# Kernel optimization log

Measured on AMD Instinct MI355X. Metric: run time of the kernel, lower is better.

The kernel has to match this reference:

```python
import jax, jax.numpy as jnp
import numpy as np

B, T, I, H, L, O = 8192, 204, 5, 24, 10, 612

def setup_inputs() -> dict:
    key = jax.random.key(0)
    ks = jax.random.split(key, 10)
    s_ih = 1.0 / np.sqrt(H)
    inp = {
        "x": jax.random.normal(ks[0], (B, T, I), dtype=jnp.float32),
        # torch nn.LSTM params: weight_ih_l0 [4H,I], weight_hh_l0 [4H,H], biases [4H]
        "W_ih": jax.random.uniform(ks[1], (4 * H, I), jnp.float32, -s_ih, s_ih),
        "W_hh": jax.random.uniform(ks[2], (4 * H, H), jnp.float32, -s_ih, s_ih),
        "b_ih": jax.random.uniform(ks[3], (4 * H,), jnp.float32, -s_ih, s_ih),
        "b_hh": jax.random.uniform(ks[4], (4 * H,), jnp.float32, -s_ih, s_ih),
        "fc0_w": jax.random.uniform(ks[5], (L, H * T), jnp.float32, -1 / np.sqrt(H * T), 1 / np.sqrt(H * T)),
        "fc0_b": jax.random.uniform(ks[6], (L,), jnp.float32, -1 / np.sqrt(H * T), 1 / np.sqrt(H * T)),
        "out_w": jax.random.uniform(ks[7], (O, L), jnp.float32, -1 / np.sqrt(L), 1 / np.sqrt(L)),
        "out_b": jax.random.uniform(ks[8], (O,), jnp.float32, -1 / np.sqrt(L), 1 / np.sqrt(L)),
    }
    return inp

def _lstm_forward(x, W_ih, W_hh, b_ih, b_hh):
    # Precompute input projections for all timesteps: [B,T,4H] -> time-major [T,B,4H]
    x_proj = jnp.einsum("bti,gi->btg", x, W_ih) + b_ih
    x_proj = jnp.swapaxes(x_proj, 0, 1)
    h0 = jnp.zeros((x.shape[0], W_hh.shape[1]), x.dtype)
    c0 = jnp.zeros_like(h0)

    def step(carry, xt):
        h, c = carry
        gates = xt + h @ W_hh.T + b_hh  # [B,4H]; torch gate order i,f,g,o
        i, f, g, o = jnp.split(gates, 4, axis=-1)
        c = jax.nn.sigmoid(f) * c + jax.nn.sigmoid(i) * jnp.tanh(g)
        h = jax.nn.sigmoid(o) * jnp.tanh(c)
        return (h, c), h

    _, hs = jax.lax.scan(step, (h0, c0), x_proj)  # hs: [T,B,H]
    return jnp.swapaxes(hs, 0, 1)  # [B,T,H]

def reference(x, W_ih, W_hh, b_ih, b_hh, fc0_w, fc0_b, out_w, out_b):
    h = _lstm_forward(x, W_ih, W_hh, b_ih, b_hh)       # [B,T,H]
    h = h.reshape(h.shape[0], -1)                       # [B, T*H]
    h = jax.nn.relu(h @ fc0_w.T + fc0_b)                # [B, L]
    return h @ out_w.T + out_b                          # [B, O]
```

## Files before the change

kernel.cpp:

```cpp
#include <hip/hip_runtime.h>
#include <math.h>

#define T_  204
#define I_  5
#define H_  24
#define L_  10
#define O_  612
#define Bsz 8192

typedef _Float16 half8 __attribute__((ext_vector_type(8)));
typedef _Float16 half2t __attribute__((ext_vector_type(2)));
typedef float    float4t __attribute__((ext_vector_type(4)));

union U16B { float4t f4; half8 h8; float f[4]; _Float16 h[8]; half2t h2[4]; };

__device__ __forceinline__ float fast_rcp(float x){ return __builtin_amdgcn_rcpf(x); }
__device__ __forceinline__ float fast_ex2(float x){ return __builtin_amdgcn_exp2f(x); }
__device__ __forceinline__ half2t pk2(float a, float b){
    return __builtin_bit_cast(half2t, __builtin_amdgcn_cvt_pkrtz(a, b));
}

#define MFMA16(a,b,c) __builtin_amdgcn_mfma_f32_16x16x32_f16((a),(b),(c),0,0,0)

#define L2E  1.44269504f
#define L2E2 2.88539008f

__device__ __forceinline__ float sigm2(float x){
    return fast_rcp(1.f + fast_ex2(x * -L2E));
}
__device__ __forceinline__ float tanh2(float x){
    return 2.f * fast_rcp(1.f + fast_ex2(x * -L2E2)) - 1.f;
}

__global__ __launch_bounds__(64)
void pack_fc0(const float* __restrict__ fc0_w, float4t* __restrict__ dst)
{
    const int t = blockIdx.x, lane = threadIdx.x;
    const int m = lane & 15, q = lane >> 4;
    U16B v;
    #pragma unroll
    for (int i = 0; i < 8; ++i) {
        const int k = 8*q + i;
        float f = (m < L_ && k < H_) ? fc0_w[m*(T_*H_) + t*H_ + k] : 0.0f;
        v.h[i] = (_Float16)f;
    }
    dst[t*64 + lane] = v.f4;
}

__global__ __launch_bounds__(64)
void lstm_mfma(const float* __restrict__ x,
               const float* __restrict__ W_ih,
               const float* __restrict__ W_hh,
               const float* __restrict__ b_ih,
               const float* __restrict__ b_hh,
               const float* __restrict__ fc0_b,
               const float* __restrict__ out_w,
               const float* __restrict__ out_b,
               const float4t* __restrict__ fc0A,
               float* __restrict__ out)
{
    __shared__ __align__(16) _Float16 hL[16*40];
    __shared__ __align__(16) _Float16 actL[16*24];

    const int lane = threadIdx.x;
    const int m = lane & 15;
    const int q = lane >> 4;
    const int elem = blockIdx.x * 16 + m;

    const float4t zf4 = {0.f, 0.f, 0.f, 0.f};

    half8 Ag[6];
    const int g0 = m & 3, ub = 6 * (m >> 2);
    #pragma unroll
    for (int T6 = 0; T6 < 6; ++T6) {
        const int srow = g0 * H_ + ub + T6;
        float w[8];
        if (q < 3) {
            const float4t* pw = (const float4t*)(W_hh + srow*H_ + 8*q);
            float4t wa = pw[0], wb = pw[1];
            #pragma unroll
            for (int i = 0; i < 4; ++i) { w[i] = wa[i]; w[4+i] = wb[i]; }
        } else {
            #pragma unroll
            for (int i = 0; i < 8; ++i) w[i] = 0.f;
            #pragma unroll
            for (int i = 0; i < I_; ++i) w[i] = W_ih[srow*I_ + i];
            w[5] = b_ih[srow] + b_hh[srow];
        }
        U16B tw;
        #pragma unroll
        for (int i = 0; i < 8; ++i) tw.h[i] = (_Float16)w[i];
        Ag[T6] = tw.h8;
    }

    const int hwAddr = m*40 + 6*q;
    const int hrAddr = m*40 + 8*q;

    const float* xp = x + (size_t)elem * (T_*I_);

    U16B B;
    if (q < 3) B.f4 = zf4;
    else {
        B.h2[0] = pk2(xp[0], xp[1]);
        B.h2[1] = pk2(xp[2], xp[3]);
        B.h2[2] = pk2(xp[4], 1.0f);
        B.h2[3] = pk2(0.f, 0.f);
    }
    float c_[6];
    #pragma unroll
    for (int s = 0; s < 6; ++s) c_[s] = 0.f;
    float4t accF = zf4;
    float4t fa = fc0A[lane];

    for (int t = 0; t < T_; ++t) {
        const int tn = (t + 1 < T_) ? t + 1 : t;
        const float4t fan = fc0A[tn*64 + lane];
        float xn0=0.f, xn1=0.f, xn2=0.f, xn3=0.f, xn4=0.f;
        if (q == 3) {
            const float* xq = xp + tn*I_;
            xn0 = xq[0]; xn1 = xq[1]; xn2 = xq[2]; xn3 = xq[3]; xn4 = xq[4];
        }

        float4t D0 = MFMA16(Ag[0], B.h8, zf4);
        float4t D1 = MFMA16(Ag[1], B.h8, zf4);
        float4t D2 = MFMA16(Ag[2], B.h8, zf4);
        float4t D3 = MFMA16(Ag[3], B.h8, zf4);
        float4t D4 = MFMA16(Ag[4], B.h8, zf4);
        float4t D5 = MFMA16(Ag[5], B.h8, zf4);

        float hh[6];
        {
            float4t D[6] = {D0, D1, D2, D3, D4, D5};
            #pragma unroll
            for (int T6 = 0; T6 < 6; ++T6) {
                const float si = sigm2(D[T6][0]);
                const float sf = sigm2(D[T6][1]);
                const float tg = tanh2(D[T6][2]);
                const float so = sigm2(D[T6][3]);
                c_[T6] = fmaf(sf, c_[T6], si * tg);
                hh[T6] = so * tanh2(c_[T6]);
            }
        }

        *(half2t*)(&hL[hwAddr])     = pk2(hh[0], hh[1]);
        *(half2t*)(&hL[hwAddr + 2]) = pk2(hh[2], hh[3]);
        *(half2t*)(&hL[hwAddr + 4]) = pk2(hh[4], hh[5]);
        __builtin_amdgcn_wave_barrier();

        if (q < 3) {
            B.f4 = *(const float4t*)(&hL[hrAddr]);
        } else {
            B.h2[0] = pk2(xn0, xn1);
            B.h2[1] = pk2(xn2, xn3);
            B.h2[2] = pk2(xn4, 1.0f);
            B.h2[3] = pk2(0.f, 0.f);
        }

        U16B fA; fA.f4 = fa;
        accF = MFMA16(fA.h8, B.h8, accF);
        fa = fan;
    }

    float av[4];
    #pragma unroll
    for (int r = 0; r < 4; ++r) {
        const int l = 4*q + r;
        const float fb = (l < L_) ? fc0_b[l] : 0.f;
        const float v = accF[r] + fb;
        av[r] = (l < L_) ? fmaxf(v, 0.f) : 0.f;
    }
    *(half2t*)(&actL[m*24 + 4*q])     = pk2(av[0], av[1]);
    *(half2t*)(&actL[m*24 + 4*q + 2]) = pk2(av[2], av[3]);
    __builtin_amdgcn_wave_barrier();

    U16B Ba;
    if (q < 2) Ba.f4 = *(const float4t*)(&actL[m*24 + q*8]);
    else       Ba.f4 = zf4;

    for (int Tt = 0; Tt < 39; ++Tt) {
        const int row = 16*Tt + m;
        float w0=0.f,w1=0.f,w2=0.f,w3=0.f,w4=0.f,w5=0.f,w6=0.f,w7=0.f;
        if (row < O_ && q < 2) {
            const float2* p2 = (const float2*)(out_w + row*L_);
            if (q == 0) {
                float2 a = p2[0], b = p2[1], cc = p2[2], dd = p2[3];
                w0=a.x; w1=a.y; w2=b.x; w3=b.y; w4=cc.x; w5=cc.y; w6=dd.x; w7=dd.y;
            } else {
                float2 a = p2[4];
                w0=a.x; w1=a.y;
            }
        }
        U16B Aw;
        Aw.h2[0] = pk2(w0,w1); Aw.h2[1] = pk2(w2,w3);
        Aw.h2[2] = pk2(w4,w5); Aw.h2[3] = pk2(w6,w7);

        float4t dd = MFMA16(Aw.h8, Ba.h8, zf4);

        const int ob = 16*Tt + 4*q;
        if (ob < O_) {
            const float4t bias = *(const float4t*)(out_b + ob);
            #pragma unroll
            for (int r = 0; r < 4; ++r) dd[r] += bias[r];
            *(float4t*)(out + (size_t)elem*O_ + ob) = dd;
        }
    }
}

extern "C" void kernel_launch(void* const* d_in, const int* in_sizes, int n_in,
                              void* d_out, int out_size, void* d_ws, size_t ws_size,
                              hipStream_t stream)
{
    const float* x     = (const float*)d_in[0];
    const float* W_ih  = (const float*)d_in[1];
    const float* W_hh  = (const float*)d_in[2];
    const float* b_ih  = (const float*)d_in[3];
    const float* b_hh  = (const float*)d_in[4];
    const float* fc0_w = (const float*)d_in[5];
    const float* fc0_b = (const float*)d_in[6];
    const float* out_w = (const float*)d_in[7];
    const float* out_b = (const float*)d_in[8];
    float* out = (float*)d_out;
    (void)ws_size;

    pack_fc0<<<dim3(T_), dim3(64), 0, stream>>>(fc0_w, (float4t*)d_ws);
    lstm_mfma<<<dim3(Bsz/16), dim3(64), 0, stream>>>(
        x, W_ih, W_hh, b_ih, b_hh, fc0_b, out_w, out_b,
        (const float4t*)d_ws, out);
}
```

Baseline: 224.4 us.

## Split LSTM gate tiles across two waves with double-buffered LDS and drop fc0 pack kernel

Each 16-element batch block now runs on two waves. Each wave computes three of the six gate MFMA tiles and half of the fc0 outputs, and the waves exchange h through a double-buffered LDS array with a workgroup barrier every timestep. The separate fc0 packing kernel is removed: fc0_w rows are read directly from global memory in fp32 and converted to f16 inside the loop, with x prefetched two steps ahead. The aim is to halve the serial per-step work on each wave's critical path. In exchange it adds a full s_barrier per timestep, scattered 2-byte LDS stores, and an in-loop fp32-to-f16 conversion of fc0 weights.

Result: no change. 224.9 us (+0.2%).

```diff
diff --git a/kernel.cpp b/kernel.cpp
--- a/kernel.cpp
+++ b/kernel.cpp
@@ -25,159 +25,164 @@
 #define L2E  1.44269504f
 #define L2E2 2.88539008f
 
-__device__ __forceinline__ float sigm2(float x){
-    return fast_rcp(1.f + fast_ex2(x * -L2E));
-}
-__device__ __forceinline__ float tanh2(float x){
-    return 2.f * fast_rcp(1.f + fast_ex2(x * -L2E2)) - 1.f;
-}
-
-__global__ __launch_bounds__(64)
-void pack_fc0(const float* __restrict__ fc0_w, float4t* __restrict__ dst)
-{
-    const int t = blockIdx.x, lane = threadIdx.x;
-    const int m = lane & 15, q = lane >> 4;
-    U16B v;
-    #pragma unroll
-    for (int i = 0; i < 8; ++i) {
-        const int k = 8*q + i;
-        float f = (m < L_ && k < H_) ? fc0_w[m*(T_*H_) + t*H_ + k] : 0.0f;
-        v.h[i] = (_Float16)f;
-    }
-    dst[t*64 + lane] = v.f4;
-}
-
-__global__ __launch_bounds__(64)
+__device__ __forceinline__ float sigm2(float x){ return fast_rcp(1.f + fast_ex2(x * -L2E)); }
+__device__ __forceinline__ float tanh2(float x){ return 2.f * fast_rcp(1.f + fast_ex2(x * -L2E2)) - 1.f; }
+
+#define STEP_BARRIER() asm volatile("s_waitcnt lgkmcnt(0)\n\ts_barrier" ::: "memory")
+
+__global__ __launch_bounds__(128)
 void lstm_mfma(const float* __restrict__ x,
                const float* __restrict__ W_ih,
                const float* __restrict__ W_hh,
                const float* __restrict__ b_ih,
                const float* __restrict__ b_hh,
+               const float* __restrict__ fc0_w,
                const float* __restrict__ fc0_b,
                const float* __restrict__ out_w,
                const float* __restrict__ out_b,
-               const float4t* __restrict__ fc0A,
                float* __restrict__ out)
 {
-    __shared__ __align__(16) _Float16 hL[16*40];
+    __shared__ __align__(16) _Float16 hL[2*16*40];
     __shared__ __align__(16) _Float16 actL[16*24];
 
-    const int lane = threadIdx.x;
+    const int tid  = threadIdx.x;
+    const int w    = tid >> 6;
+    const int lane = tid & 63;
     const int m = lane & 15;
     const int q = lane >> 4;
     const int elem = blockIdx.x * 16 + m;
 
     const float4t zf4 = {0.f, 0.f, 0.f, 0.f};
 
-    half8 Ag[6];
+    half8 Ag[3];
     const int g0 = m & 3, ub = 6 * (m >> 2);
     #pragma unroll
-    for (int T6 = 0; T6 < 6; ++T6) {
-        const int srow = g0 * H_ + ub + T6;
-        float w[8];
+    for (int T3 = 0; T3 < 3; ++T3) {
+        const int gT = 3*w + T3;
+        const int srow = g0 * H_ + ub + gT;
+        float wv[8];
         if (q < 3) {
             const float4t* pw = (const float4t*)(W_hh + srow*H_ + 8*q);
             float4t wa = pw[0], wb = pw[1];
             #pragma unroll
-            for (int i = 0; i < 4; ++i) { w[i] = wa[i]; w[4+i] = wb[i]; }
+            for (int i = 0; i < 4; ++i) { wv[i] = wa[i]; wv[4+i] = wb[i]; }
         } else {
             #pragma unroll
-            for (int i = 0; i < 8; ++i) w[i] = 0.f;
-            #pragma unroll
-            for (int i = 0; i < I_; ++i) w[i] = W_ih[srow*I_ + i];
-            w[5] = b_ih[srow] + b_hh[srow];
+            for (int i = 0; i < 8; ++i) wv[i] = 0.f;
+            #pragma unroll
+            for (int i = 0; i < I_; ++i) wv[i] = W_ih[srow*I_ + i];
+            wv[5] = b_ih[srow] + b_hh[srow];
         }
         U16B tw;
         #pragma unroll
-        for (int i = 0; i < 8; ++i) tw.h[i] = (_Float16)w[i];
-        Ag[T6] = tw.h8;
-    }
-
-    const int hwAddr = m*40 + 6*q;
-    const int hrAddr = m*40 + 8*q;
+        for (int i = 0; i < 8; ++i) tw.h[i] = (_Float16)wv[i];
+        Ag[T3] = tw.h8;
+    }
+
+    const int hwIdx = m*40 + 6*q + 3*w;
+    const int hrIdx = m*40 + 8*q;
 
     const float* xp = x + (size_t)elem * (T_*I_);
 
+    const bool fval = (m < 5) && (q < 3);
+    const float* fbase = fc0_w + (size_t)(5*w + (m < 5 ? m : 0)) * (T_*H_) + 8*q;
+    float4t fA0 = zf4, fA1 = zf4;
+    if (fval) {
+        fA0 = *(const float4t*)(fbase + 0);
+        fA1 = *(const float4t*)(fbase + 4);
+    }
+
+    float xA0=0,xA1=0,xA2=0,xA3=0,xA4=0;
     U16B B;
-    if (q < 3) B.f4 = zf4;
-    else {
+    if (q == 3) {
         B.h2[0] = pk2(xp[0], xp[1]);
         B.h2[1] = pk2(xp[2], xp[3]);
         B.h2[2] = pk2(xp[4], 1.0f);
         B.h2[3] = pk2(0.f, 0.f);
-    }
-    float c_[6];
-    #pragma unroll
-    for (int s = 0; s < 6; ++s) c_[s] = 0.f;
+        xA0 = xp[I_+0]; xA1 = xp[I_+1]; xA2 = xp[I_+2]; xA3 = xp[I_+3]; xA4 = xp[I_+4];
+    } else {
+        B.f4 = zf4;
+    }
+
+    float c_[3] = {0.f, 0.f, 0.f};
     float4t accF = zf4;
-    float4t fa = fc0A[lane];
-
+
+    #pragma unroll 2
     for (int t = 0; t < T_; ++t) {
-        const int tn = (t + 1 < T_) ? t + 1 : t;
-        const float4t fan = fc0A[tn*64 + lane];
-        float xn0=0.f, xn1=0.f, xn2=0.f, xn3=0.f, xn4=0.f;
+        float xB0=0,xB1=0,xB2=0,xB3=0,xB4=0;
         if (q == 3) {
-            const float* xq = xp + tn*I_;
-            xn0 = xq[0]; xn1 = xq[1]; xn2 = xq[2]; xn3 = xq[3]; xn4 = xq[4];
+            const int tp2 = (t + 2 < T_) ? t + 2 : T_ - 1;
+            const float* xq = xp + tp2*I_;
+            xB0 = xq[0]; xB1 = xq[1]; xB2 = xq[2]; xB3 = xq[3]; xB4 = xq[4];
+        }
+        float4t fB0 = zf4, fB1 = zf4;
+        {
+            const int tp1 = (t + 1 < T_) ? t + 1 : T_ - 1;
+            if (fval) {
+                fB0 = *(const float4t*)(fbase + tp1*H_ + 0);
+                fB1 = *(const float4t*)(fbase + tp1*H_ + 4);
+            }
         }
 
         float4t D0 = MFMA16(Ag[0], B.h8, zf4);
         float4t D1 = MFMA16(Ag[1], B.h8, zf4);
         float4t D2 = MFMA16(Ag[2], B.h8, zf4);
-        float4t D3 = MFMA16(Ag[3], B.h8, zf4);
-        float4t D4 = MFMA16(Ag[4], B.h8, zf4);
-        float4t D5 = MFMA16(Ag[5], B.h8, zf4);
-
-        float hh[6];
+
+        const int bofs = (t & 1) * 640;
         {
-            float4t D[6] = {D0, D1, D2, D3, D4, D5};
-            #pragma unroll
-            for (int T6 = 0; T6 < 6; ++T6) {
-                const float si = sigm2(D[T6][0]);
-                const float sf = sigm2(D[T6][1]);
-                const float tg = tanh2(D[T6][2]);
-                const float so = sigm2(D[T6][3]);
-                c_[T6] = fmaf(sf, c_[T6], si * tg);
-                hh[T6] = so * tanh2(c_[T6]);
+            float4t D[3] = {D0, D1, D2};
+            #pragma unroll
+            for (int T3 = 0; T3 < 3; ++T3) {
+                const float si = sigm2(D[T3][0]);
+                const float sf = sigm2(D[T3][1]);
+                const float tg = tanh2(D[T3][2]);
+                const float so = sigm2(D[T3][3]);
+                c_[T3] = fmaf(sf, c_[T3], si * tg);
+                const float hh = so * tanh2(c_[T3]);
+                hL[bofs + hwIdx + T3] = (_Float16)hh;
             }
         }
 
-        *(half2t*)(&hL[hwAddr])     = pk2(hh[0], hh[1]);
-        *(half2t*)(&hL[hwAddr + 2]) = pk2(hh[2], hh[3]);
-        *(half2t*)(&hL[hwAddr + 4]) = pk2(hh[4], hh[5]);
-        __builtin_amdgcn_wave_barrier();
+        STEP_BARRIER();
 
         if (q < 3) {
-            B.f4 = *(const float4t*)(&hL[hrAddr]);
+            B.f4 = *(const float4t*)(&hL[bofs + hrIdx]);
         } else {
-            B.h2[0] = pk2(xn0, xn1);
-            B.h2[1] = pk2(xn2, xn3);
-            B.h2[2] = pk2(xn4, 1.0f);
+            B.h2[0] = pk2(xA0, xA1);
+            B.h2[1] = pk2(xA2, xA3);
+            B.h2[2] = pk2(xA4, 1.0f);
             B.h2[3] = pk2(0.f, 0.f);
         }
 
-        U16B fA; fA.f4 = fa;
-        accF = MFMA16(fA.h8, B.h8, accF);
-        fa = fan;
-    }
-
-    float av[4];
+        U16B fF;
+        fF.h2[0] = pk2(fA0[0], fA0[1]);
+        fF.h2[1] = pk2(fA0[2], fA0[3]);
+        fF.h2[2] = pk2(fA1[0], fA1[1]);
+        fF.h2[3] = pk2(fA1[2], fA1[3]);
+        accF = MFMA16(fF.h8, B.h8, accF);
+
+        fA0 = fB0; fA1 = fB1;
+        xA0 = xB0; xA1 = xB1; xA2 = xB2; xA3 = xB3; xA4 = xB4;
+    }
+
     #pragma unroll
     for (int r = 0; r < 4; ++r) {
-        const int l = 4*q + r;
-        const float fb = (l < L_) ? fc0_b[l] : 0.f;
-        const float v = accF[r] + fb;
-        av[r] = (l < L_) ? fmaxf(v, 0.f) : 0.f;
-    }
-    *(half2t*)(&actL[m*24 + 4*q])     = pk2(av[0], av[1]);
-    *(half2t*)(&actL[m*24 + 4*q + 2]) = pk2(av[2], av[3]);
-    __builtin_amdgcn_wave_barrier();
+        const int rid = 4*q + r;
+        if (rid < 5) {
+            const int l = 5*w + rid;
+            const float v = accF[r] + fc0_b[l];
+            actL[m*24 + l] = (_Float16)fmaxf(v, 0.f);
+        } else if (w == 0 && rid >= 10) {
+            actL[m*24 + rid] = (_Float16)0.f;
+        }
+    }
+    __syncthreads();
 
     U16B Ba;
-    if (q < 2) Ba.f4 = *(const float4t*)(&actL[m*24 + q*8]);
+    if (q < 2) Ba.f4 = *(const float4t*)(&actL[m*24 + 8*q]);
     else       Ba.f4 = zf4;
 
-    for (int Tt = 0; Tt < 39; ++Tt) {
+    for (int Tt = w; Tt < 39; Tt += 2) {
         const int row = 16*Tt + m;
         float w0=0.f,w1=0.f,w2=0.f,w3=0.f,w4=0.f,w5=0.f,w6=0.f,w7=0.f;
         if (row < O_ && q < 2) {
@@ -220,10 +225,8 @@
     const float* out_w = (const float*)d_in[7];
     const float* out_b = (const float*)d_in[8];
     float* out = (float*)d_out;
-    (void)ws_size;
-
-    pack_fc0<<<dim3(T_), dim3(64), 0, stream>>>(fc0_w, (float4t*)d_ws);
-    lstm_mfma<<<dim3(Bsz/16), dim3(64), 0, stream>>>(
-        x, W_ih, W_hh, b_ih, b_hh, fc0_b, out_w, out_b,
-        (const float4t*)d_ws, out);
+    (void)d_ws; (void)ws_size;
+
+    lstm_mfma<<<dim3(Bsz/16), dim3(128), 0, stream>>>(
+        x, W_ih, W_hh, b_ih, b_hh, fc0_w, fc0_b, out_w, out_b, out);
 }
```

## Remap LSTM hidden units to lanes and exchange h via shuffles instead of LDS

Applied to the files above, without the earlier changes.

The assignment of hidden units to MFMA output lanes is remapped so that each lane's own computed h values land directly in the positions of its next-step B operand. Only two units per lane group now come from another lane, and those arrive through a cross-lane shuffle. This removes the per-step LDS write, wave barrier and LDS read from the serial recurrence. The input x is also prefetched two steps ahead instead of one to hide global-load latency. The shuffles still go through the LDS crossbar, so the latency saved on the critical path may be small.

Result: no change. 221.1 us (-1.5%).

```diff
diff --git a/kernel.cpp b/kernel.cpp
--- a/kernel.cpp
+++ b/kernel.cpp
@@ -25,11 +25,11 @@
 #define L2E  1.44269504f
 #define L2E2 2.88539008f
 
-__device__ __forceinline__ float sigm2(float x){
-    return fast_rcp(1.f + fast_ex2(x * -L2E));
-}
-__device__ __forceinline__ float tanh2(float x){
-    return 2.f * fast_rcp(1.f + fast_ex2(x * -L2E2)) - 1.f;
+__device__ __forceinline__ float sigm2(float x){ return fast_rcp(1.f + fast_ex2(x * -L2E)); }
+__device__ __forceinline__ float tanh2(float x){ return 2.f * fast_rcp(1.f + fast_ex2(x * -L2E2)) - 1.f; }
+
+__device__ __forceinline__ int unit_of(int q, int T) {
+    return (q < 3) ? (8*q + T) : (8*(T >> 1) + 6 + (T & 1));
 }
 
 __global__ __launch_bounds__(64)
@@ -59,7 +59,6 @@
                const float4t* __restrict__ fc0A,
                float* __restrict__ out)
 {
-    __shared__ __align__(16) _Float16 hL[16*40];
     __shared__ __align__(16) _Float16 actL[16*24];
 
     const int lane = threadIdx.x;
@@ -70,55 +69,59 @@
     const float4t zf4 = {0.f, 0.f, 0.f, 0.f};
 
     half8 Ag[6];
-    const int g0 = m & 3, ub = 6 * (m >> 2);
     #pragma unroll
     for (int T6 = 0; T6 < 6; ++T6) {
-        const int srow = g0 * H_ + ub + T6;
-        float w[8];
+        const int u = unit_of(m >> 2, T6);
+        const int srow = (m & 3) * H_ + u;
+        float wv[8];
         if (q < 3) {
             const float4t* pw = (const float4t*)(W_hh + srow*H_ + 8*q);
             float4t wa = pw[0], wb = pw[1];
             #pragma unroll
-            for (int i = 0; i < 4; ++i) { w[i] = wa[i]; w[4+i] = wb[i]; }
+            for (int i = 0; i < 4; ++i) { wv[i] = wa[i]; wv[4+i] = wb[i]; }
         } else {
             #pragma unroll
-            for (int i = 0; i < 8; ++i) w[i] = 0.f;
-            #pragma unroll
-            for (int i = 0; i < I_; ++i) w[i] = W_ih[srow*I_ + i];
-            w[5] = b_ih[srow] + b_hh[srow];
+            for (int i = 0; i < 8; ++i) wv[i] = 0.f;
+            #pragma unroll
+            for (int i = 0; i < I_; ++i) wv[i] = W_ih[srow*I_ + i];
+            wv[5] = b_ih[srow] + b_hh[srow];
         }
         U16B tw;
         #pragma unroll
-        for (int i = 0; i < 8; ++i) tw.h[i] = (_Float16)w[i];
+        for (int i = 0; i < 8; ++i) tw.h[i] = (_Float16)wv[i];
         Ag[T6] = tw.h8;
     }
 
-    const int hwAddr = m*40 + 6*q;
-    const int hrAddr = m*40 + 8*q;
-
     const float* xp = x + (size_t)elem * (T_*I_);
 
     U16B B;
-    if (q < 3) B.f4 = zf4;
-    else {
+    if (q == 3) {
         B.h2[0] = pk2(xp[0], xp[1]);
         B.h2[1] = pk2(xp[2], xp[3]);
         B.h2[2] = pk2(xp[4], 1.0f);
         B.h2[3] = pk2(0.f, 0.f);
-    }
-    float c_[6];
-    #pragma unroll
-    for (int s = 0; s < 6; ++s) c_[s] = 0.f;
+    } else {
+        B.f4 = zf4;
+    }
+    float xC[I_] = {0,0,0,0,0};
+    if (q == 3) {
+        #pragma unroll
+        for (int i = 0; i < I_; ++i) xC[i] = xp[I_ + i];
+    }
+
+    float c_[6] = {0,0,0,0,0,0};
     float4t accF = zf4;
     float4t fa = fc0A[lane];
 
     for (int t = 0; t < T_; ++t) {
         const int tn = (t + 1 < T_) ? t + 1 : t;
         const float4t fan = fc0A[tn*64 + lane];
-        float xn0=0.f, xn1=0.f, xn2=0.f, xn3=0.f, xn4=0.f;
+        float xN[I_] = {0,0,0,0,0};
         if (q == 3) {
-            const float* xq = xp + tn*I_;
-            xn0 = xq[0]; xn1 = xq[1]; xn2 = xq[2]; xn3 = xq[3]; xn4 = xq[4];
+            const int tp2 = (t + 2 < T_) ? t + 2 : T_ - 1;
+            const float* xq = xp + tp2*I_;
+            #pragma unroll
+            for (int i = 0; i < I_; ++i) xN[i] = xq[i];
         }
 
         float4t D0 = MFMA16(Ag[0], B.h8, zf4);
@@ -142,23 +145,34 @@
             }
         }
 
-        *(half2t*)(&hL[hwAddr])     = pk2(hh[0], hh[1]);
-        *(half2t*)(&hL[hwAddr + 2]) = pk2(hh[2], hh[3]);
-        *(half2t*)(&hL[hwAddr + 4]) = pk2(hh[4], hh[5]);
-        __builtin_amdgcn_wave_barrier();
+        const float P0 = __builtin_bit_cast(float, pk2(hh[0], hh[1]));
+        const float P1 = __builtin_bit_cast(float, pk2(hh[2], hh[3]));
+        const float P2 = __builtin_bit_cast(float, pk2(hh[4], hh[5]));
+
+        const int src = 48 + m;
+        const float r0 = __shfl(P0, src, 64);
+        const float r1 = __shfl(P1, src, 64);
+        const float r2 = __shfl(P2, src, 64);
+        const float rcv = (q == 0) ? r0 : ((q == 1) ? r1 : r2);
 
         if (q < 3) {
-            B.f4 = *(const float4t*)(&hL[hrAddr]);
+            B.h2[0] = __builtin_bit_cast(half2t, P0);
+            B.h2[1] = __builtin_bit_cast(half2t, P1);
+            B.h2[2] = __builtin_bit_cast(half2t, P2);
+            B.h2[3] = __builtin_bit_cast(half2t, rcv);
         } else {
-            B.h2[0] = pk2(xn0, xn1);
-            B.h2[1] = pk2(xn2, xn3);
-            B.h2[2] = pk2(xn4, 1.0f);
+            B.h2[0] = pk2(xC[0], xC[1]);
+            B.h2[1] = pk2(xC[2], xC[3]);
+            B.h2[2] = pk2(xC[4], 1.0f);
             B.h2[3] = pk2(0.f, 0.f);
         }
 
-        U16B fA; fA.f4 = fa;
-        accF = MFMA16(fA.h8, B.h8, accF);
+        U16B fF; fF.f4 = fa;
+        accF = MFMA16(fF.h8, B.h8, accF);
+
         fa = fan;
+        #pragma unroll
+        for (int i = 0; i < I_; ++i) xC[i] = xN[i];
     }
 
     float av[4];
```
